# Kernel tuning notes

Hardware: AMD Instinct MI355X
Metric: run time of the kernel (lower is better)

## Reference

```python
import jax, jax.numpy as jnp
import numpy as np

B, D, PRE, NXT, J, K, A = 1000, 8, 98, 2048, 32, 64, 5

def setup_inputs() -> dict:
    key = jax.random.key(0)
    ks = jax.random.split(key, 20)
    s = 0.05  # weight scale to keep activations sane
    inp = {
        'x': jax.random.normal(ks[0], (B, D * PRE), jnp.float32),
        'W1': jax.random.normal(ks[1], (D, NXT, PRE), jnp.float32) * s,
        'b1': jax.random.normal(ks[2], (D, NXT), jnp.float32) * s,
        'Wc': jax.random.normal(ks[3], (D, J, NXT), jnp.float32) * s,
        'bc': jax.random.normal(ks[4], (D, J), jnp.float32) * s,
        'cut_layer_bias': jax.random.normal(ks[5], (J,), jnp.float32) * s,
        'b_mat': jax.random.normal(ks[6], (D, J), jnp.float32) * s,
        'h_mat': jax.random.normal(ks[7], (D, K, A), jnp.float32),
        'a_mat': jax.random.normal(ks[8], (J, A), jnp.float32) * s,
        'noise': jax.random.normal(ks[9], (J, A), jnp.float32),  # tau2 = 1.0
        'W3': jax.random.normal(ks[10], (98, J), jnp.float32) * s,
        'b3': jax.random.normal(ks[11], (98,), jnp.float32) * s,
        'W4': jax.random.normal(ks[12], (49, 98), jnp.float32) * s,
        'b4': jax.random.normal(ks[13], (49,), jnp.float32) * s,
        'Wo': jax.random.normal(ks[14], (10, 49), jnp.float32) * s,
        'bo': jax.random.normal(ks[15], (10,), jnp.float32) * s,
    }
    # one-hot subcarrier allocation: each symbol j assigned exactly one subcarrier k
    assign = jax.random.randint(ks[16], (J,), 0, K)
    inp['indicator'] = jax.nn.one_hot(assign, K, dtype=jnp.float32)
    return inp


def reference(x, W1, b1, Wc, bc, cut_layer_bias, b_mat, h_mat, a_mat, indicator,
              noise, W3, b3, W4, b4, Wo, bo):
    b = x.shape[0]
    xs = x.reshape(b, D, PRE)                                   # split across devices
    sub = jax.nn.relu(jnp.einsum('bdi,doi->bdo', xs, W1) + b1)  # [B,D,NXT]
    # online cross-device mean/var via .item() in torch => stats are non-differentiable scalars
    m = jnp.mean(sub, axis=(0, 2))                              # per-device mean [D]
    v = jnp.mean((sub - m[None, :, None]) ** 2, axis=(0, 2))    # per-device var  [D]
    gm = jax.lax.stop_gradient(jnp.mean(m))
    gv = jax.lax.stop_gradient(jnp.mean(v))
    norm = (sub - gm) / jnp.sqrt(gv + 1e-6)
    dso = jnp.einsum('bdo,djo->bdj', norm, Wc) + bc             # device-side outputs [B,D,J]
    # channel: gather assigned subcarrier per symbol, combine with receive beamformers a_j
    h_sel = jnp.einsum('jk,nkd->njd', indicator, h_mat)         # [D,J,A]
    h_vec = jnp.einsum('njd,jd->nj', h_sel, a_mat)              # [D,J]
    received = jnp.einsum('bnj,nj->bj', dso * b_mat[None], h_vec)  # [B,J]
    received = received + jnp.sum(a_mat * noise, axis=1)[None, :]  # scaled noise per symbol
    h = jax.nn.relu(received + cut_layer_bias)
    h = jax.nn.relu(h @ W3.T + b3)
    h = jax.nn.relu(h @ W4.T + b4)
    return jax.nn.log_softmax(h @ Wo.T + bo, axis=1)
```

## Files before the change

### kernel.cpp

```cpp
#include <hip/hip_runtime.h>
#include <math.h>

#define B_ 1000
#define D_ 8
#define PRE_ 98
#define NXT_ 2048
#define J_ 32
#define K_ 64
#define A_ 5

typedef __attribute__((ext_vector_type(8))) __bf16 bf16x8;
typedef __attribute__((ext_vector_type(4))) float f32x4;
typedef __attribute__((ext_vector_type(16))) float f32x16;
typedef __attribute__((ext_vector_type(8))) unsigned short us8;

__device__ __forceinline__ unsigned cvtpk(float lo, float hi) {
  unsigned r;
  asm("v_cvt_pk_bf16_f32 %0, %1, %2" : "=v"(r) : "v"(lo), "v"(hi));
  return r;
}

union bfu { unsigned u[4]; bf16x8 v; };


__global__ __launch_bounds__(256) void kcvt(
    const float* __restrict__ x, const float* __restrict__ W1,
    const float* __restrict__ b1, const float* __restrict__ Wc,
    const float* __restrict__ h_mat, const float* __restrict__ a_mat,
    const float* __restrict__ noise, const float* __restrict__ indicator,
    unsigned short* __restrict__ w1a, unsigned short* __restrict__ xa,
    unsigned short* __restrict__ wca, float* __restrict__ wcp,
    float* __restrict__ hvec, float* __restrict__ nz) {
  __shared__ float sbuf[32 * 257];
  __shared__ float extra[32];
  __shared__ float ws2[32][9];

  const int bid = blockIdx.x, tid = threadIdx.x;

  if (bid < 512) {
    const int d = bid & 7, og = bid >> 3;
    const float* base = W1 + (size_t)3136 * (d * 64 + og);
    for (int idx = tid; idx < 784; idx += 256) {
      float4 v4 = ((const float4*)base)[idx];
      int p = idx * 4;
      const float vv[4] = {v4.x, v4.y, v4.z, v4.w};
#pragma unroll
      for (int e = 0; e < 4; ++e) {
        int pp = p + e;
        int r = pp / 98, k = pp - r * 98;
        sbuf[r * 99 + k] = vv[e];
      }
    }
    if (tid < 32) extra[tid] = b1[d * NXT_ + og * 32 + tid];
    __syncthreads();
    unsigned short* dst = w1a + (size_t)((d * 64 + og) * 7) * 512;
#pragma unroll
    for (int q = 0; q < 2; ++q) {
      int s = tid + q * 256;
      if (s < 448) {
        int ks = s >> 6, l = s & 63;
        int r = l & 31, k0 = ks * 16 + (l >> 5) * 8;
        const float* row = sbuf + r * 99;
        bfu v;
#pragma unroll
        for (int p = 0; p < 4; ++p) {
          int k = k0 + 2 * p;
          float f0 = (k < 98) ? row[k] : ((k == 98) ? extra[r] : 0.0f);
          float f1 = (k + 1 < 98) ? row[k + 1] : ((k + 1 == 98) ? extra[r] : 0.0f);
          v.u[p] = cvtpk(f0, f1);
        }
        *(bf16x8*)(dst + (size_t)s * 8) = v.v;
      }
    }
  } else if (bid < 768) {
    const int b2 = bid - 512;
    const int d = b2 & 7, bg = b2 >> 3;
    for (int idx = tid; idx < 1568; idx += 256) {
      int r = idx / 49, c = idx - r * 49;
      int gb = bg * 32 + r;
      float2 v2 = make_float2(0.0f, 0.0f);
      if (gb < B_)
        v2 = *(const float2*)(x + (size_t)gb * (D_ * PRE_) + d * PRE_ + 2 * c);
      sbuf[r * 99 + 2 * c] = v2.x;
      sbuf[r * 99 + 2 * c + 1] = v2.y;
    }
    __syncthreads();
    unsigned short* dst = xa + (size_t)((d * 32 + bg) * 7) * 512;
#pragma unroll
    for (int q = 0; q < 2; ++q) {
      int s = tid + q * 256;
      if (s < 448) {
        int ks = s >> 6, l = s & 63;
        int r = l & 31, k0 = ks * 16 + (l >> 5) * 8;
        bool valid = (bg * 32 + r) < B_;
        const float* row = sbuf + r * 99;
        bfu v;
#pragma unroll
        for (int p = 0; p < 4; ++p) {
          int k = k0 + 2 * p;
          float f0 = 0.0f, f1 = 0.0f;
          if (valid) {
            f0 = (k < 98) ? row[k] : ((k == 98) ? 1.0f : 0.0f);
            f1 = (k + 1 < 98) ? row[k + 1] : ((k + 1 == 98) ? 1.0f : 0.0f);
          }
          v.u[p] = cvtpk(f0, f1);
        }
        *(bf16x8*)(dst + (size_t)s * 8) = v.v;
      }
    }
  } else if (bid < 832) {
    const int b3 = bid - 768;
    const int d = b3 & 7, oq = b3 >> 3;
    for (int idx = tid; idx < 2048; idx += 256) {
      int j = idx >> 6, c = idx & 63;
      float4 v4 = *(const float4*)(Wc + ((size_t)d * J_ + j) * NXT_ +
                                   oq * 256 + 4 * c);
      float* p = sbuf + j * 257 + 4 * c;
      p[0] = v4.x;
      p[1] = v4.y;
      p[2] = v4.z;
      p[3] = v4.w;
    }
    __syncthreads();
    unsigned short* dst = wca + (size_t)((d * 64 + oq * 8) * 2) * 512;
#pragma unroll
    for (int q = 0; q < 4; ++q) {
      int s = tid + q * 256;
      int ogl = s >> 7, t2 = (s >> 6) & 1, l = s & 63;
      int j = l & 31;
      int ol = ogl * 32 + t2 * 16 + (l >> 5) * 8;
      const float* row = sbuf + j * 257 + ol;
      bfu v;
#pragma unroll
      for (int p = 0; p < 4; ++p) v.u[p] = cvtpk(row[2 * p], row[2 * p + 1]);
      *(bf16x8*)(dst + (size_t)s * 8) = v.v;
    }
    {
      int j = tid >> 3, seg = tid & 7;
      const float* row = sbuf + j * 257 + seg * 32;
      float sacc = 0.0f;
#pragma unroll
      for (int i = 0; i < 32; ++i) sacc += row[i];
      ws2[j][seg] = sacc;
    }
    __syncthreads();
    if (tid < 32) {
      float t = 0.0f;
#pragma unroll
      for (int g = 0; g < 8; ++g) t += ws2[tid][g];
      wcp[((size_t)d * 32 + tid) * 8 + oq] = t;
    }
  } else {
    int dd = tid >> 5, j = tid & 31;
    float hs[A_] = {0, 0, 0, 0, 0};
    for (int k = 0; k < K_; ++k) {
      float indv = indicator[j * K_ + k];
      if (indv != 0.0f) {
        const float* hp = h_mat + ((size_t)dd * K_ + k) * A_;
#pragma unroll
        for (int a = 0; a < A_; ++a) hs[a] = fmaf(indv, hp[a], hs[a]);
      }
    }
    float hv = 0.0f;
#pragma unroll
    for (int a = 0; a < A_; ++a) hv = fmaf(hs[a], a_mat[j * A_ + a], hv);
    hvec[tid] = hv;
    if (tid < J_) {
      float nzv = 0.0f;
#pragma unroll
      for (int a = 0; a < A_; ++a)
        nzv = fmaf(a_mat[tid * A_ + a], noise[tid * A_ + a], nzv);
      nz[tid] = nzv;
    }
  }
}

__global__ __launch_bounds__(256, 4) void k1(
    const unsigned short* __restrict__ w1a,
    const unsigned short* __restrict__ xa,
    const unsigned short* __restrict__ wca, float* __restrict__ S1part,
    float* __restrict__ spsum, float* __restrict__ spsq) {
  __shared__ float red[4][32 * 33];

  const int id = blockIdx.x;
  const int d = id & 7;
  const int r2 = id >> 3;
  const int bg = r2 & 31, oc = r2 >> 5;
  const int tid = threadIdx.x;
  const int w = tid >> 6, lane = tid & 63;
  const int l31 = lane & 31, hi = lane >> 5;
  const bool lo_half = (hi == 0);

  bf16x8 xf[7];
  {
    const unsigned short* xb =
        xa + (size_t)((d * 32 + bg) * 7) * 512 + lane * 8;
#pragma unroll
    for (int ks = 0; ks < 7; ++ks) xf[ks] = *(const bf16x8*)(xb + ks * 512);
  }

  f32x16 acc2 = {};
  float lsum = 0.0f, lsq = 0.0f;

#pragma unroll 2
  for (int i = 0; i < 4; ++i) {
    const int og = oc * 16 + w * 4 + i;
    const unsigned short* ab =
        w1a + (size_t)((d * 64 + og) * 7) * 512 + lane * 8;
    const unsigned short* wb =
        wca + (size_t)((d * 64 + og) * 2) * 512 + lane * 8;
    bf16x8 wc0 = *(const bf16x8*)(wb);
    bf16x8 wc1 = *(const bf16x8*)(wb + 512);

    f32x16 acc = {};
#pragma unroll
    for (int ks = 0; ks < 7; ++ks) {
      bf16x8 a = *(const bf16x8*)(ab + ks * 512);
      acc = __builtin_amdgcn_mfma_f32_32x32x16_bf16(a, xf[ks], acc, 0, 0, 0);
    }

    float v[16];
#pragma unroll
    for (int r = 0; r < 16; ++r) {
      v[r] = fmaxf(acc[r], 0.0f);
      lsum += v[r];
      lsq = fmaf(v[r], v[r], lsq);
    }
#pragma unroll
    for (int t = 0; t < 2; ++t) {
      unsigned A0 = cvtpk(v[8 * t + 0], v[8 * t + 1]);
      unsigned A1 = cvtpk(v[8 * t + 2], v[8 * t + 3]);
      unsigned B0 = cvtpk(v[8 * t + 4], v[8 * t + 5]);
      unsigned B1 = cvtpk(v[8 * t + 6], v[8 * t + 7]);
      unsigned sA0 = __shfl_xor(A0, 32);
      unsigned sA1 = __shfl_xor(A1, 32);
      unsigned sB0 = __shfl_xor(B0, 32);
      unsigned sB1 = __shfl_xor(B1, 32);
      bfu f;
      f.u[0] = lo_half ? A0 : sB0;
      f.u[1] = lo_half ? A1 : sB1;
      f.u[2] = lo_half ? sA0 : B0;
      f.u[3] = lo_half ? sA1 : B1;
      acc2 = __builtin_amdgcn_mfma_f32_32x32x16_bf16(t == 0 ? wc0 : wc1, f.v,
                                                     acc2, 0, 0, 0);
    }
  }

  {
    float* tw = red[w];
#pragma unroll
    for (int r = 0; r < 16; ++r) {
      int j = (r & 3) + 8 * (r >> 2) + 4 * hi;
      tw[l31 * 33 + j] = acc2[r];
    }
  }
  __syncthreads();

  {
    const int row = tid >> 3, j0 = (tid & 7) * 4;
    f32x4 s;
#pragma unroll
    for (int e = 0; e < 4; ++e) {
      float acc_ = 0.0f;
#pragma unroll
      for (int ww = 0; ww < 4; ++ww) acc_ += red[ww][row * 33 + j0 + e];
      s[e] = acc_;
    }
    const int b = bg * 32 + row;
    *(f32x4*)(S1part + (((size_t)oc * 1024 + b) * 8 + d) * 32 + j0) = s;
  }

#pragma unroll
  for (int off = 32; off; off >>= 1) {
    lsum += __shfl_down(lsum, off);
    lsq += __shfl_down(lsq, off);
  }
  if (lane == 0) {
    spsum[id * 4 + w] = lsum;
    spsq[id * 4 + w] = lsq;
  }
}

#define W3S 33
#define W4S 99

__global__ __launch_bounds__(256) void kB(
    const float* __restrict__ S1part, const float* __restrict__ spsum,
    const float* __restrict__ spsq, const float* __restrict__ wcp,
    const float* __restrict__ hvec, const float* __restrict__ nz,
    const float* __restrict__ bc, const float* __restrict__ b_mat,
    const float* __restrict__ cutb, const float* __restrict__ W3,
    const float* __restrict__ b3, const float* __restrict__ W4,
    const float* __restrict__ b4, const float* __restrict__ Wo,
    const float* __restrict__ bo, float* __restrict__ out) {
  __shared__ float W3l[98 * W3S];
  __shared__ float W4l[49 * W4S];
  __shared__ float Wol[490];
  __shared__ float b3l[98], b4l[49], bol[10];
  __shared__ float cutl[32], coefl[256], konstl[32], wcs[256];
  __shared__ float psum[8][33], psq[8][33];
  __shared__ float mvals[8], vvals[8];
  __shared__ float sh_gm, sh_inv;
  __shared__ float offs[D_][J_];
  __shared__ float h1[4][32];
  __shared__ float h2[4][100];
  __shared__ float h3[4][52];
  __shared__ float lg[4][10];
  __shared__ float lsel[4];

  const int tid = threadIdx.x;

  for (int idx = tid; idx < 784; idx += 256) {
    float4 v4 = ((const float4*)W3)[idx];
    int p = idx * 4;
    const float vv[4] = {v4.x, v4.y, v4.z, v4.w};
#pragma unroll
    for (int e = 0; e < 4; ++e) {
      int pp = p + e;
      W3l[(pp >> 5) * W3S + (pp & 31)] = vv[e];
    }
  }
  for (int idx = tid; idx < 2401; idx += 256) {
    float2 v2 = ((const float2*)W4)[idx];
    int p = idx * 2;
    int o = p / 98, k = p - o * 98;
    W4l[o * W4S + k] = v2.x;
    W4l[o * W4S + k + 1] = v2.y;
  }
  if (tid < 245) {
    float2 v2 = ((const float2*)Wo)[tid];
    Wol[2 * tid] = v2.x;
    Wol[2 * tid + 1] = v2.y;
  }
  if (tid < 49) {
    float2 v2 = ((const float2*)b3)[tid];
    b3l[2 * tid] = v2.x;
    b3l[2 * tid + 1] = v2.y;
    b4l[tid] = b4[tid];
  }
  if (tid < 10) bol[tid] = bo[tid];
  if (tid < 32) cutl[tid] = cutb[tid];

  {
    const float4* p = (const float4*)(wcp + (size_t)tid * 8);
    float4 a = p[0], b = p[1];
    wcs[tid] = a.x + a.y + a.z + a.w + b.x + b.y + b.z + b.w;
  }

  {
    int dd = tid >> 5, i = tid & 31;
    float s = 0.0f, q = 0.0f;
#pragma unroll
    for (int m = 0; m < 4; ++m) {
      int k = i + m * 32;
      int base = (k * 8 + dd) * 4;
#pragma unroll
      for (int ww = 0; ww < 4; ++ww) {
        s += spsum[base + ww];
        q += spsq[base + ww];
      }
    }
    psum[dd][i] = s;
    psq[dd][i] = q;
  }
  __syncthreads();
  if (tid < 8) {
    float s = 0.0f, q = 0.0f;
#pragma unroll
    for (int i = 0; i < 32; ++i) {
      s += psum[tid][i];
      q += psq[tid][i];
    }
    const float inv_cnt = 1.0f / ((float)B_ * (float)NXT_);
    float m = s * inv_cnt;
    mvals[tid] = m;
    vvals[tid] = q * inv_cnt - m * m;
  }
  __syncthreads();
  if (tid == 0) {
    float gm = 0.0f, gv = 0.0f;
    for (int dd = 0; dd < 8; ++dd) {
      gm += mvals[dd];
      gv += vvals[dd];
    }
    gm *= 0.125f;
    gv *= 0.125f;
    sh_gm = gm;
    sh_inv = 1.0f / sqrtf(gv + 1e-6f);
  }
  __syncthreads();
  {
    int dd = tid >> 5, j = tid & 31;
    float c = b_mat[dd * J_ + j] * hvec[tid];
    coefl[tid] = c * sh_inv;
    offs[dd][j] = c * (bc[dd * J_ + j] - sh_gm * wcs[tid] * sh_inv);
  }
  __syncthreads();
  if (tid < J_) {
    float s = nz[tid];
#pragma unroll
    for (int dd = 0; dd < D_; ++dd) s += offs[dd][tid];
    konstl[tid] = s;
  }
  __syncthreads();

  const int row = tid >> 6, lane = tid & 63;
  const int b = blockIdx.x * 4 + row;

  if (lane < 32) {
    float rsum = konstl[lane];
#pragma unroll
    for (int dd = 0; dd < D_; ++dd) {
      float s = 0.0f;
#pragma unroll
      for (int p = 0; p < 4; ++p)
        s += S1part[(((size_t)p * 1024 + b) * 8 + dd) * 32 + lane];
      rsum = fmaf(coefl[dd * J_ + lane], s, rsum);
    }
    h1[row][lane] = fmaxf(rsum + cutl[lane], 0.0f);
  }
  __syncthreads();

  for (int o = lane; o < 98; o += 64) {
    float a = b3l[o];
#pragma unroll
    for (int j = 0; j < 32; ++j) a = fmaf(h1[row][j], W3l[o * W3S + j], a);
    h2[row][o] = fmaxf(a, 0.0f);
  }
  __syncthreads();

  if (lane < 49) {
    float a = b4l[lane];
    for (int k = 0; k < 98; ++k)
      a = fmaf(h2[row][k], W4l[lane * W4S + k], a);
    h3[row][lane] = fmaxf(a, 0.0f);
  }
  __syncthreads();

  if (lane < 10) {
    float a = bol[lane];
#pragma unroll
    for (int k = 0; k < 49; ++k) a = fmaf(h3[row][k], Wol[lane * 49 + k], a);
    lg[row][lane] = a;
  }
  __syncthreads();
  if (lane == 0) {
    float mx = lg[row][0];
    for (int i = 1; i < 10; ++i) mx = fmaxf(mx, lg[row][i]);
    float se = 0.0f;
    for (int i = 0; i < 10; ++i) se += expf(lg[row][i] - mx);
    lsel[row] = mx + logf(se);
  }
  __syncthreads();
  if (lane < 10) out[(size_t)b * 10 + lane] = lg[row][lane] - lsel[row];
}

extern "C" void kernel_launch(void* const* d_in, const int* in_sizes, int n_in,
                              void* d_out, int out_size, void* d_ws,
                              size_t ws_size, hipStream_t stream) {
  const float* x = (const float*)d_in[0];
  const float* W1 = (const float*)d_in[1];
  const float* b1 = (const float*)d_in[2];
  const float* Wc = (const float*)d_in[3];
  const float* bc = (const float*)d_in[4];
  const float* cutb = (const float*)d_in[5];
  const float* bmat = (const float*)d_in[6];
  const float* hmat = (const float*)d_in[7];
  const float* amat = (const float*)d_in[8];
  const float* noise = (const float*)d_in[9];
  const float* W3 = (const float*)d_in[10];
  const float* b3 = (const float*)d_in[11];
  const float* W4 = (const float*)d_in[12];
  const float* b4 = (const float*)d_in[13];
  const float* Wo = (const float*)d_in[14];
  const float* bo = (const float*)d_in[15];
  const float* ind = (const float*)d_in[16];

  float* ws = (float*)d_ws;
  float* S1part = ws;
  unsigned short* w1a = (unsigned short*)(ws + 1048576);
  unsigned short* xa = (unsigned short*)(ws + 1966080);
  unsigned short* wca = (unsigned short*)(ws + 2424832);
  float* spsum = ws + 2686976;
  float* spsq = ws + 2691072;
  float* wcp = ws + 2695168;
  float* hvec = ws + 2697216;
  float* nz = ws + 2697472;

  kcvt<<<833, 256, 0, stream>>>(x, W1, b1, Wc, hmat, amat, noise, ind, w1a,
                                xa, wca, wcp, hvec, nz);
  k1<<<1024, 256, 0, stream>>>(w1a, xa, wca, S1part, spsum, spsq);
  kB<<<250, 256, 0, stream>>>(S1part, spsum, spsq, wcp, hvec, nz, bc, bmat,
                              cutb, W3, b3, W4, b4, Wo, bo, (float*)d_out);
}
```

Baseline: 38.26 us.

## Stage W1/Wc tiles in LDS via direct global-to-LDS loads, share across batch halves

k1 now runs 512 threads per block covering two 32-row batch tiles that share one set of W1/Wc weight fragments. The fragments are staged into 72KB of dynamic LDS with global_load_lds, so each fragment is fetched once per block instead of once per warp. The output-channel split doubles from 4 to 8 partitions, so S1part and the stat partials grow and kB sums 8 partials instead of 4. The cost is a large LDS footprint that limits occupancy, an extra barrier before compute, and more partial-sum traffic in kB.

```diff
diff --git a/kernel.cpp b/kernel.cpp
--- a/kernel.cpp
+++ b/kernel.cpp
@@ -18,6 +18,12 @@
   unsigned r;
   asm("v_cvt_pk_bf16_f32 %0, %1, %2" : "=v"(r) : "v"(lo), "v"(hi));
   return r;
+}
+
+__device__ __forceinline__ void gload16(const void* g, void* l) {
+  __builtin_amdgcn_global_load_lds(
+      (const __attribute__((address_space(1))) void*)g,
+      (__attribute__((address_space(3))) void*)l, 16, 0, 0);
 }
 
 union bfu { unsigned u[4]; bf16x8 v; };
@@ -175,47 +181,61 @@
   }
 }
 
-__global__ __launch_bounds__(256, 4) void k1(
+__global__ __launch_bounds__(512, 4) void k1(
     const unsigned short* __restrict__ w1a,
     const unsigned short* __restrict__ xa,
     const unsigned short* __restrict__ wca, float* __restrict__ S1part,
     float* __restrict__ spsum, float* __restrict__ spsq) {
-  __shared__ float red[4][32 * 33];
+  extern __shared__ __align__(16) char smem[];
 
   const int id = blockIdx.x;
   const int d = id & 7;
-  const int r2 = id >> 3;
-  const int bg = r2 & 31, oc = r2 >> 5;
+  const int rest = id >> 3;
+  const int bt = rest & 15, oc = rest >> 4;
   const int tid = threadIdx.x;
   const int w = tid >> 6, lane = tid & 63;
+  const int bh = w >> 2, q = w & 3;
   const int l31 = lane & 31, hi = lane >> 5;
   const bool lo_half = (hi == 0);
 
+  {
+    const unsigned short* w1src =
+        w1a + ((size_t)d * 448 + oc * 56) * 512 + lane * 8;
+    const unsigned short* wcsrc =
+        wca + ((size_t)d * 128 + oc * 16) * 512 + lane * 8;
+#pragma unroll
+    for (int c = 0; c < 9; ++c) {
+      int f = w * 9 + c;
+      const unsigned short* src = (f < 56) ? (w1src + (size_t)f * 512)
+                                           : (wcsrc + (size_t)(f - 56) * 512);
+      gload16(src, smem + (size_t)f * 1024);
+    }
+  }
+
   bf16x8 xf[7];
   {
     const unsigned short* xb =
-        xa + (size_t)((d * 32 + bg) * 7) * 512 + lane * 8;
+        xa + (size_t)((d * 32 + bt * 2 + bh) * 7) * 512 + lane * 8;
 #pragma unroll
     for (int ks = 0; ks < 7; ++ks) xf[ks] = *(const bf16x8*)(xb + ks * 512);
   }
+  __syncthreads();
 
   f32x16 acc2 = {};
   float lsum = 0.0f, lsq = 0.0f;
 
-#pragma unroll 2
-  for (int i = 0; i < 4; ++i) {
-    const int og = oc * 16 + w * 4 + i;
-    const unsigned short* ab =
-        w1a + (size_t)((d * 64 + og) * 7) * 512 + lane * 8;
-    const unsigned short* wb =
-        wca + (size_t)((d * 64 + og) * 2) * 512 + lane * 8;
+#pragma unroll
+  for (int i2 = 0; i2 < 2; ++i2) {
+    const int ogl = q * 2 + i2;
+    const char* ab = smem + (size_t)(ogl * 7) * 1024 + lane * 16;
+    const char* wb = smem + (size_t)(56 + ogl * 2) * 1024 + lane * 16;
     bf16x8 wc0 = *(const bf16x8*)(wb);
-    bf16x8 wc1 = *(const bf16x8*)(wb + 512);
+    bf16x8 wc1 = *(const bf16x8*)(wb + 1024);
 
     f32x16 acc = {};
 #pragma unroll
     for (int ks = 0; ks < 7; ++ks) {
-      bf16x8 a = *(const bf16x8*)(ab + ks * 512);
+      bf16x8 a = *(const bf16x8*)(ab + (size_t)ks * 1024);
       acc = __builtin_amdgcn_mfma_f32_32x32x16_bf16(a, xf[ks], acc, 0, 0, 0);
     }
 
@@ -246,27 +266,31 @@
     }
   }
 
-  {
-    float* tw = red[w];
+  __syncthreads();
+  float* redf = (float*)smem;
+  {
 #pragma unroll
     for (int r = 0; r < 16; ++r) {
       int j = (r & 3) + 8 * (r >> 2) + 4 * hi;
-      tw[l31 * 33 + j] = acc2[r];
-    }
-  }
-  __syncthreads();
-
-  {
-    const int row = tid >> 3, j0 = (tid & 7) * 4;
+      redf[(bh * 4 + q) * 1056 + l31 * 33 + j] = acc2[r];
+    }
+  }
+  __syncthreads();
+
+  {
+    const int half = tid >> 8;
+    const int row = (tid >> 3) & 31;
+    const int j0 = (tid & 7) * 4;
     f32x4 s;
 #pragma unroll
     for (int e = 0; e < 4; ++e) {
       float acc_ = 0.0f;
 #pragma unroll
-      for (int ww = 0; ww < 4; ++ww) acc_ += red[ww][row * 33 + j0 + e];
+      for (int ww = 0; ww < 4; ++ww)
+        acc_ += redf[(half * 4 + ww) * 1056 + row * 33 + j0 + e];
       s[e] = acc_;
     }
-    const int b = bg * 32 + row;
+    const int b = (bt * 2 + half) * 32 + row;
     *(f32x4*)(S1part + (((size_t)oc * 1024 + b) * 8 + d) * 32 + j0) = s;
   }
 
@@ -276,8 +300,8 @@
     lsq += __shfl_down(lsq, off);
   }
   if (lane == 0) {
-    spsum[id * 4 + w] = lsum;
-    spsq[id * 4 + w] = lsq;
+    spsum[id * 8 + w] = lsum;
+    spsq[id * 8 + w] = lsq;
   }
 }
 
@@ -352,10 +376,10 @@
     float s = 0.0f, q = 0.0f;
 #pragma unroll
     for (int m = 0; m < 4; ++m) {
-      int k = i + m * 32;
-      int base = (k * 8 + dd) * 4;
-#pragma unroll
-      for (int ww = 0; ww < 4; ++ww) {
+      int rest = i + m * 32;
+      int base = (rest * 8 + dd) * 8;
+#pragma unroll
+      for (int ww = 0; ww < 8; ++ww) {
         s += spsum[base + ww];
         q += spsq[base + ww];
       }
@@ -413,7 +437,7 @@
     for (int dd = 0; dd < D_; ++dd) {
       float s = 0.0f;
 #pragma unroll
-      for (int p = 0; p < 4; ++p)
+      for (int p = 0; p < 8; ++p)
         s += S1part[(((size_t)p * 1024 + b) * 8 + dd) * 32 + lane];
       rsum = fmaf(coefl[dd * J_ + lane], s, rsum);
     }
@@ -478,18 +502,18 @@
 
   float* ws = (float*)d_ws;
   float* S1part = ws;
-  unsigned short* w1a = (unsigned short*)(ws + 1048576);
-  unsigned short* xa = (unsigned short*)(ws + 1966080);
-  unsigned short* wca = (unsigned short*)(ws + 2424832);
-  float* spsum = ws + 2686976;
-  float* spsq = ws + 2691072;
-  float* wcp = ws + 2695168;
-  float* hvec = ws + 2697216;
-  float* nz = ws + 2697472;
+  unsigned short* w1a = (unsigned short*)(ws + 2097152);
+  unsigned short* xa = (unsigned short*)(ws + 2555904);
+  unsigned short* wca = (unsigned short*)(ws + 2785280);
+  float* spsum = ws + 3047424;
+  float* spsq = ws + 3055616;
+  float* wcp = ws + 3063808;
+  float* hvec = ws + 3065856;
+  float* nz = ws + 3066112;
 
   kcvt<<<833, 256, 0, stream>>>(x, W1, b1, Wc, hmat, amat, noise, ind, w1a,
                                 xa, wca, wcp, hvec, nz);
-  k1<<<1024, 256, 0, stream>>>(w1a, xa, wca, S1part, spsum, spsq);
+  k1<<<1024, 512, 73728, stream>>>(w1a, xa, wca, S1part, spsum, spsq);
   kB<<<250, 256, 0, stream>>>(S1part, spsum, spsq, wcp, hvec, nz, bc, bmat,
                               cutb, W3, b3, W4, b4, Wo, bo, (float*)d_out);
 }
```

Measured after the change: 45.56 us. 1.19x slower.
